# Kernel optimization log

Hardware: AMD Instinct MI355X
Metric: run time of the kernel (lower is better)

The kernel has to match this reference:

```python
import jax, jax.numpy as jnp
import numpy as np

N, E, DIM, L, NPERM, B = 20000, 640000, 128, 4, 20000, 256
R = NPERM * L * L  # rows of perm matrices
EPS = 1e-5


def _mlp(x, w1, b1, g, beta, w2, b2):
    # Linear -> BatchNorm (training-mode batch stats) -> ReLU -> Linear
    h = x @ w1 + b1
    mu = h.mean(0)
    var = h.var(0)  # biased, matches torch BN normalization
    h = (h - mu) * jax.lax.rsqrt(var + EPS) * g + beta
    return jax.nn.relu(h) @ w2 + b2


def setup_inputs() -> dict:
    key = jax.random.key(0)
    ks = jax.random.split(key, 40)
    s = 0.05
    inp = {}
    inp["node_feat"] = jax.random.normal(ks[0], (N, DIM), jnp.float32)
    inp["edge_feat"] = jax.random.normal(ks[1], (E, DIM), jnp.float32)
    inp["src"] = jax.random.randint(ks[2], (E,), 0, N)
    inp["dst"] = jax.random.randint(ks[3], (E,), 0, N)
    inp["rev_flag"] = jax.random.randint(ks[4], (E,), 0, 2).astype(bool)
    # sparse node_to_perm / edge_to_perm: one nnz per row (row i implicit)
    inp["n2p_cols"] = jax.random.randint(ks[5], (R,), 0, N)
    inp["n2p_vals"] = jax.random.uniform(ks[6], (R,), jnp.float32)
    inp["e2p_cols"] = jax.random.randint(ks[7], (R,), 0, E)
    inp["e2p_vals"] = jax.random.uniform(ks[8], (R,), jnp.float32)
    # sparse pooling matrix: perm j -> graph pool_rows[j] with weight pool_vals[j]
    inp["pool_rows"] = jax.random.randint(ks[9], (NPERM,), 0, B)
    inp["pool_vals"] = jax.random.uniform(ks[10], (NPERM,), jnp.float32)
    for i, n in enumerate(["in_w", "out_w", "src_w", "dst_w", "nloop_w", "eloop_w"]):
        inp[n] = jax.random.normal(ks[11 + i], (DIM, DIM), jnp.float32) * s
    inp["lrp_w"] = jax.random.normal(ks[17], (DIM, DIM, L * L), jnp.float32) * s
    inp["nbias"] = jnp.zeros((DIM,), jnp.float32)
    inp["ebias"] = jnp.zeros((DIM,), jnp.float32)
    inp["lrp_bias"] = jnp.zeros((DIM,), jnp.float32)
    for p, k0 in (("n", 20), ("e", 26)):
        inp[p + "mlp_w1"] = jax.random.normal(ks[k0], (DIM, DIM), jnp.float32) * s
        inp[p + "mlp_b1"] = jnp.zeros((DIM,), jnp.float32)
        inp[p + "mlp_g"] = jnp.ones((DIM,), jnp.float32)
        inp[p + "mlp_beta"] = jnp.zeros((DIM,), jnp.float32)
        inp[p + "mlp_w2"] = jax.random.normal(ks[k0 + 1], (DIM, DIM), jnp.float32) * s
        inp[p + "mlp_b2"] = jnp.zeros((DIM,), jnp.float32)
    return inp


def reference(node_feat, edge_feat, src, dst, rev_flag, n2p_cols, n2p_vals,
              e2p_cols, e2p_vals, pool_rows, pool_vals,
              in_w, out_w, src_w, dst_w, nloop_w, eloop_w, lrp_w,
              nbias, ebias, lrp_bias,
              nmlp_w1, nmlp_b1, nmlp_g, nmlp_beta, nmlp_w2, nmlp_b2,
              emlp_w1, emlp_b1, emlp_g, emlp_beta, emlp_w2, emlp_b2):
    hs = node_feat[src]   # [E, d]
    hd = node_feat[dst]   # [E, d]
    r = rev_flag[:, None]
    # per-edge messages with reverse-edge masking
    edge_msg = jnp.where(r, hs @ dst_w - hd @ src_w, hd @ dst_w - hs @ src_w)
    node_msg = jnp.where(r, edge_feat @ out_w, -(edge_feat @ in_w))
    node_agg = jax.ops.segment_sum(node_msg, dst, num_segments=N)
    # node update
    nout = _mlp(node_feat @ nloop_w + node_agg + nbias,
                nmlp_w1, nmlp_b1, nmlp_g, nmlp_beta, nmlp_w2, nmlp_b2)
    # edge update: degree-scaled term uses out-degree of dst node
    out_deg = jax.ops.segment_sum(jnp.ones((E,), jnp.float32), src, num_segments=N)
    dlog = jnp.log2(1.0 + out_deg[dst])[:, None]
    add = 2.0 * (1.0 + dlog) * (edge_feat @ (src_w - dst_w))
    eout = _mlp(edge_feat @ eloop_w + add + edge_msg + ebias,
                emlp_w1, emlp_b1, emlp_g, emlp_beta, emlp_w2, emlp_b2)
    # sparse perm gathers + LRP einsum + sparse pooling scatter
    perm = n2p_vals[:, None] * nout[n2p_cols] + e2p_vals[:, None] * eout[e2p_cols]
    perm = perm.reshape(NPERM, L * L, DIM)
    lrp = jnp.einsum('dab,bca->dc', perm, lrp_w) + lrp_bias
    pooled = jax.ops.segment_sum(pool_vals[:, None] * lrp, pool_rows, num_segments=B)
    return pooled, eout
```

## Files before the change

kernel.cpp:

```cpp
#include <hip/hip_runtime.h>
#include <stdint.h>

constexpr int Nn     = 20000;
constexpr int Ee     = 640000;
constexpr int NPERMc = 20000;

using bf16x8 = __attribute__((ext_vector_type(8))) short;
using f32x4  = __attribute__((ext_vector_type(4))) float;
using s16x4  = __attribute__((ext_vector_type(4))) short;
using u16x8  = __attribute__((ext_vector_type(8))) unsigned short;

__device__ __forceinline__ short f2bf(float f) {
  union { float f; unsigned u; } v; v.f = f;
  unsigned r = v.u + 0x7FFFu + ((v.u >> 16) & 1u);
  return (short)(r >> 16);
}
__device__ __forceinline__ float bf2f(unsigned short s) {
  union { unsigned u; float f; } v; v.u = ((unsigned)s) << 16;
  return v.f;
}
__device__ __forceinline__ f32x4 MFMA(bf16x8 a, bf16x8 b, f32x4 c) {
  return __builtin_amdgcn_mfma_f32_16x16x32_bf16(a, b, c, 0, 0, 0);
}

__device__ __forceinline__ int swz(int s) { return s ^ (((s >> 7) & 7) << 3); }

__device__ __forceinline__ int fragIdx(int k, int n) {
  int t = n >> 4, kk = k >> 5;
  int l = ((k & 31) >> 3) * 16 + (n & 15);
  int j = k & 7;
  return ((t * 4 + kk) * 64 + l) * 8 + j;
}

__device__ __forceinline__ void stage16x128(const float* __restrict__ src, int row0, int M,
                                            int lane, short* lds) {
  #pragma unroll
  for (int it = 0; it < 8; ++it) {
    int u = it * 64 + lane;
    int r = u >> 5;
    int q = u & 31;
    int row = row0 + r;
    float4 v = make_float4(0.f, 0.f, 0.f, 0.f);
    if (row < M) v = ((const float4*)(src + (size_t)row * 128))[q];
    int k  = q * 4;
    int kk = k >> 5;
    int l2 = ((k & 31) >> 3) * 16 + r;
    int j  = k & 7;
    s16x4 s4 = { f2bf(v.x), f2bf(v.y), f2bf(v.z), f2bf(v.w) };
    *(s16x4*)(lds + swz((kk * 64 + l2) * 8 + j)) = s4;
  }
}

__global__ __launch_bounds__(256) void kPrep(
    const float* __restrict__ in_w,  const float* __restrict__ out_w,
    const float* __restrict__ src_w, const float* __restrict__ dst_w,
    const float* __restrict__ nloop_w, const float* __restrict__ eloop_w,
    const float* __restrict__ lrp_w,
    const float* __restrict__ nbias, const float* __restrict__ ebias,
    const float* __restrict__ w1e, const float* __restrict__ b1e,
    const float* __restrict__ w1n, const float* __restrict__ b1n,
    const float* __restrict__ w2e, const float* __restrict__ w2n,
    short* __restrict__ WA, short* __restrict__ BQ, short* __restrict__ WN,
    short* __restrict__ W2E, short* __restrict__ W2N, short* __restrict__ WL,
    float* __restrict__ c0e, float* __restrict__ c0n) {
  __shared__ float Rl[16384];
  int tid = threadIdx.x;
  int blk = blockIdx.x;
  if (blk < 448) {
    int p = blk >> 6, sub = blk & 63;
    const float* La; const float* Lb = nullptr; const float* R; short* outp;
    float sOut = 1.f;
    switch (p) {
      case 0: La = eloop_w;             R = w1e; outp = WA;          break;
      case 1: La = src_w; Lb = dst_w;   R = w1e; outp = WA + 16384;  break;
      case 2: La = dst_w;               R = w1e; outp = BQ;          break;
      case 3: La = src_w;               R = w1e; outp = BQ + 16384;  break;
      case 4: La = nloop_w;             R = w1n; outp = WN;          break;
      case 5: La = out_w;               R = w1n; outp = WN + 16384;  break;
      default: La = in_w;               R = w1n; outp = WN + 32768; sOut = -1.f; break;
    }
    for (int i = tid; i < 16384; i += 256) Rl[i] = R[i];
    __syncthreads();
    int e = sub * 256 + tid;
    int k = e >> 7, n = e & 127;
    float acc = 0.f;
    bool hasLb = (Lb != nullptr);
    for (int j = 0; j < 128; ++j) {
      float l = La[k * 128 + j];
      if (hasLb) l -= Lb[k * 128 + j];
      acc += l * Rl[j * 128 + n];
    }
    outp[fragIdx(k, n)] = f2bf(acc * sOut);
  } else if (blk < 512) {
    int e = (blk - 448) * 256 + tid; int k = e >> 7, n = e & 127;
    W2E[fragIdx(k, n)] = f2bf(w2e[k * 128 + n]);
  } else if (blk < 576) {
    int e = (blk - 512) * 256 + tid; int k = e >> 7, n = e & 127;
    W2N[fragIdx(k, n)] = f2bf(w2n[k * 128 + n]);
  } else if (blk < 1600) {
    int q = blk - 576; int a = q >> 6;
    int e = (q & 63) * 256 + tid; int k = e >> 7, n = e & 127;
    WL[a * 16384 + fragIdx(k, n)] = f2bf(lrp_w[(k * 128 + n) * 16 + a]);
  } else {
    if (tid < 128) {
      float acc = 0.f;
      for (int k2 = 0; k2 < 128; ++k2) acc += ebias[k2] * w1e[k2 * 128 + tid];
      c0e[tid] = acc + b1e[tid];
    } else {
      int n = tid - 128; float acc = 0.f;
      for (int k2 = 0; k2 < 128; ++k2) acc += nbias[k2] * w1n[k2 * 128 + n];
      c0n[n] = acc + b1n[n];
    }
  }
}


__global__ __launch_bounds__(256) void kHist(
    const int* __restrict__ srcI, const int* __restrict__ dstI,
    int* __restrict__ cnt, float* __restrict__ deg) {
  int e = blockIdx.x * 256 + threadIdx.x;
  atomicAdd(&cnt[dstI[e]], 1);
  atomicAdd(&deg[srcI[e]], 1.0f);
}

__global__ __launch_bounds__(256) void kScan(const int* __restrict__ cnt,
                                             int* __restrict__ off,
                                             int* __restrict__ cur) {
  __shared__ int lc[Nn];
  __shared__ int ps[256];
  int tid = threadIdx.x;
  for (int i = tid; i < Nn; i += 256) lc[i] = cnt[i];
  __syncthreads();
  constexpr int CH = (Nn + 255) / 256;
  int base = tid * CH;
  int local = 0;
  for (int i = 0; i < CH; ++i) {
    int idx = base + i;
    if (idx < Nn) local += lc[idx];
  }
  ps[tid] = local;
  __syncthreads();
  for (int d = 1; d < 256; d <<= 1) {
    int t = (tid >= d) ? ps[tid - d] : 0;
    __syncthreads();
    if (tid >= d) ps[tid] += t;
    __syncthreads();
  }
  int run = ps[tid] - local;
  for (int i = 0; i < CH; ++i) {
    int idx = base + i;
    if (idx < Nn) { off[idx] = run; cur[idx] = run; run += lc[idx]; }
  }
}

__global__ __launch_bounds__(256) void kScatter(
    const int* __restrict__ dstI, const int* __restrict__ revI,
    int* __restrict__ cur, int* __restrict__ order) {
  int e = blockIdx.x * 256 + threadIdx.x;
  int pos = atomicAdd(&cur[dstI[e]], 1);
  order[pos] = revI[e] ? (e | (int)0x80000000) : e;
}

__global__ __launch_bounds__(256) void kAgg2(
    const float* __restrict__ ef, const int* __restrict__ off,
    const int* __restrict__ cnt, const int* __restrict__ order,
    float* __restrict__ aggR, float* __restrict__ aggN) {
  int w = threadIdx.x >> 6, lane = threadIdx.x & 63;
  int n = blockIdx.x * 4 + w;
  if (n >= Nn) return;
  int s0 = off[n], c = cnt[n];
  float2 aR = make_float2(0.f, 0.f), aN = make_float2(0.f, 0.f);
  int i = 0;
  for (; i + 3 < c; i += 4) {
    int oe0 = order[s0 + i];
    int oe1 = order[s0 + i + 1];
    int oe2 = order[s0 + i + 2];
    int oe3 = order[s0 + i + 3];
    float2 v0 = ((const float2*)(ef + (size_t)(oe0 & 0x7fffffff) * 128))[lane];
    float2 v1 = ((const float2*)(ef + (size_t)(oe1 & 0x7fffffff) * 128))[lane];
    float2 v2 = ((const float2*)(ef + (size_t)(oe2 & 0x7fffffff) * 128))[lane];
    float2 v3 = ((const float2*)(ef + (size_t)(oe3 & 0x7fffffff) * 128))[lane];
    if (oe0 < 0) { aR.x += v0.x; aR.y += v0.y; } else { aN.x += v0.x; aN.y += v0.y; }
    if (oe1 < 0) { aR.x += v1.x; aR.y += v1.y; } else { aN.x += v1.x; aN.y += v1.y; }
    if (oe2 < 0) { aR.x += v2.x; aR.y += v2.y; } else { aN.x += v2.x; aN.y += v2.y; }
    if (oe3 < 0) { aR.x += v3.x; aR.y += v3.y; } else { aN.x += v3.x; aN.y += v3.y; }
  }
  for (; i < c; ++i) {
    int oe = order[s0 + i];
    int e = oe & 0x7fffffff;
    float2 v = ((const float2*)(ef + (size_t)e * 128))[lane];
    if (oe < 0) { aR.x += v.x; aR.y += v.y; } else { aN.x += v.x; aN.y += v.y; }
  }
  ((float2*)(aggR + (size_t)n * 128))[lane] = aR;
  ((float2*)(aggN + (size_t)n * 128))[lane] = aN;
}

__global__ __launch_bounds__(256, 2) void kQ(const float* __restrict__ nf,
                                             const short* __restrict__ BQ,
                                             float* __restrict__ Q, int M) {
  __shared__ __align__(16) short alds[4][2048];
  __shared__ __align__(16) short wbuf[8192];
  int tid = threadIdx.x, w = tid >> 6, lane = tid & 63;
  int row0 = blockIdx.x * 64 + w * 16;
  stage16x128(nf, row0, M, lane, alds[w]);
  f32x4 acc[16];
  #pragma unroll
  for (int t = 0; t < 16; ++t) acc[t] = (f32x4){0.f, 0.f, 0.f, 0.f};
  const int4* g4 = (const int4*)BQ;
  for (int kk = 0; kk < 4; ++kk) {
    __syncthreads();
    for (int c = tid; c < 1024; c += 256) {
      int t = c >> 6, l = c & 63;
      ((int4*)wbuf)[c] = g4[(t * 4 + kk) * 64 + l];
    }
    __syncthreads();
    bf16x8 a = *(const bf16x8*)(alds[w] + swz((kk * 64 + lane) * 8));
    #pragma unroll
    for (int t = 0; t < 16; ++t) {
      bf16x8 b = *(const bf16x8*)(wbuf + (t * 64 + lane) * 8);
      acc[t] = MFMA(a, b, acc[t]);
    }
  }
  int sub = lane >> 4, m = lane & 15;
  #pragma unroll
  for (int i = 0; i < 4; ++i) {
    int row = row0 + sub * 4 + i;
    if (row < M) {
      #pragma unroll
      for (int h = 0; h < 2; ++h) {
        float4 f0, f1;
        f0.x = acc[h * 8 + 0][i]; f0.y = acc[h * 8 + 1][i];
        f0.z = acc[h * 8 + 2][i]; f0.w = acc[h * 8 + 3][i];
        f1.x = acc[h * 8 + 4][i]; f1.y = acc[h * 8 + 5][i];
        f1.z = acc[h * 8 + 6][i]; f1.w = acc[h * 8 + 7][i];
        float4* dst = (float4*)(Q + (size_t)row * 256 + h * 128 + m * 8);
        dst[0] = f0; dst[1] = f1;
      }
    }
  }
}

__global__ __launch_bounds__(256, 2) void kN1(
    const float* __restrict__ nf, const float* __restrict__ aggR,
    const float* __restrict__ aggN, const short* __restrict__ WN,
    const float* __restrict__ c0n, short* __restrict__ hN,
    float* __restrict__ scratchN, int M) {
  __shared__ __align__(16) short alds[4][2048];
  __shared__ __align__(16) short wlds[16384];
  __shared__ float statsLDS[256];
  int tid = threadIdx.x, w = tid >> 6, lane = tid & 63;
  int m = lane & 15, sub = lane >> 4;
  statsLDS[tid] = 0.f;
  int row0 = blockIdx.x * 64 + w * 16;
  f32x4 acc[8];
  #pragma unroll
  for (int t = 0; t < 8; ++t) acc[t] = (f32x4){0.f, 0.f, 0.f, 0.f};
  for (int s = 0; s < 3; ++s) {
    const float* src = (s == 0) ? nf : ((s == 1) ? aggR : aggN);
    __syncthreads();
    const int4* g4 = (const int4*)(WN + s * 16384);
    for (int c = tid; c < 2048; c += 256) ((int4*)wlds)[c] = g4[c];
    __syncthreads();
    stage16x128(src, row0, M, lane, alds[w]);
    for (int kk = 0; kk < 4; ++kk) {
      bf16x8 a = *(const bf16x8*)(alds[w] + swz((kk * 64 + lane) * 8));
      #pragma unroll
      for (int t = 0; t < 8; ++t) {
        bf16x8 b = *(const bf16x8*)(wlds + ((t * 4 + kk) * 64 + lane) * 8);
        acc[t] = MFMA(a, b, acc[t]);
      }
    }
  }
  float c0v[8];
  #pragma unroll
  for (int t = 0; t < 8; ++t) c0v[t] = c0n[t * 16 + m];
  float ss[8], sq[8];
  #pragma unroll
  for (int t = 0; t < 8; ++t) { ss[t] = 0.f; sq[t] = 0.f; }
  #pragma unroll
  for (int i = 0; i < 4; ++i) {
    int row = row0 + sub * 4 + i;
    if (row < M) {
      bf16x8 pk;
      #pragma unroll
      for (int t = 0; t < 8; ++t) {
        float h = acc[t][i] + c0v[t];
        pk[t] = f2bf(h); ss[t] += h; sq[t] += h * h;
      }
      *(bf16x8*)(hN + (size_t)row * 128 + m * 8) = pk;
    }
  }
  #pragma unroll
  for (int t = 0; t < 8; ++t) {
    float a = ss[t], b = sq[t];
    a += __shfl_xor(a, 16, 64); b += __shfl_xor(b, 16, 64);
    a += __shfl_xor(a, 32, 64); b += __shfl_xor(b, 32, 64);
    if (lane < 16) {
      atomicAdd(&statsLDS[t * 16 + lane], a);
      atomicAdd(&statsLDS[128 + t * 16 + lane], b);
    }
  }
  __syncthreads();
  scratchN[(size_t)blockIdx.x * 256 + tid] = statsLDS[tid];
}

__global__ __launch_bounds__(256, 4) void kD(
    const float* __restrict__ ef, const short* __restrict__ WA,
    const float* __restrict__ Q, const float* __restrict__ c0e,
    const int* __restrict__ srcI, const int* __restrict__ dstI,
    const int* __restrict__ revI, const float* __restrict__ deg,
    short* __restrict__ hE, float* __restrict__ scratchE) {
  __shared__ __align__(16) short alds[4][2048];
  __shared__ __align__(16) short wbuf[8192];
  __shared__ float statsLDS[256];
  int tid = threadIdx.x, w = tid >> 6, lane = tid & 63;
  int m = lane & 15, sub = lane >> 4;
  statsLDS[tid] = 0.f;
  int row0 = blockIdx.x * 64 + w * 16;
  float scl[4]; int qa[4], qb[4];
  #pragma unroll
  for (int i = 0; i < 4; ++i) {
    int e = row0 + sub * 4 + i;
    int s_ = srcI[e], d_ = dstI[e], r_ = revI[e];
    scl[i] = 2.0f * (1.0f + log2f(1.0f + deg[d_]));
    int na = r_ ? s_ : d_;
    int nb = r_ ? d_ : s_;
    qa[i] = na * 256 + m * 8;
    qb[i] = nb * 256 + 128 + m * 8;
  }
  stage16x128(ef, row0, Ee, lane, alds[w]);
  f32x4 acc1[8], acc2[8];
  #pragma unroll
  for (int t = 0; t < 8; ++t) { acc1[t] = (f32x4){0,0,0,0}; acc2[t] = (f32x4){0,0,0,0}; }
  const int4* g4 = (const int4*)WA;
  for (int kk = 0; kk < 4; ++kk) {
    __syncthreads();
    for (int c = tid; c < 1024; c += 256) {
      int mm = c >> 9, t = (c >> 6) & 7, l = c & 63;
      ((int4*)wbuf)[c] = g4[mm * 2048 + (t * 4 + kk) * 64 + l];
    }
    __syncthreads();
    bf16x8 a = *(const bf16x8*)(alds[w] + swz((kk * 64 + lane) * 8));
    #pragma unroll
    for (int t = 0; t < 8; ++t) {
      bf16x8 b1 = *(const bf16x8*)(wbuf + (t * 64 + lane) * 8);
      bf16x8 b2 = *(const bf16x8*)(wbuf + 4096 + (t * 64 + lane) * 8);
      acc1[t] = MFMA(a, b1, acc1[t]);
      acc2[t] = MFMA(a, b2, acc2[t]);
    }
  }
  float c0v[8];
  #pragma unroll
  for (int t = 0; t < 8; ++t) c0v[t] = c0e[t * 16 + m];
  float ss[8], sq[8];
  #pragma unroll
  for (int t = 0; t < 8; ++t) { ss[t] = 0.f; sq[t] = 0.f; }
  #pragma unroll
  for (int i = 0; i < 4; ++i) {
    int e = row0 + sub * 4 + i;
    float4 A0 = ((const float4*)(Q + qa[i]))[0];
    float4 A1 = ((const float4*)(Q + qa[i]))[1];
    float4 B0 = ((const float4*)(Q + qb[i]))[0];
    float4 B1 = ((const float4*)(Q + qb[i]))[1];
    float qv[8] = {A0.x - B0.x, A0.y - B0.y, A0.z - B0.z, A0.w - B0.w,
                   A1.x - B1.x, A1.y - B1.y, A1.z - B1.z, A1.w - B1.w};
    bf16x8 pk;
    #pragma unroll
    for (int t = 0; t < 8; ++t) {
      float h = acc1[t][i] + scl[i] * acc2[t][i] + qv[t] + c0v[t];
      pk[t] = f2bf(h);
      ss[t] += h; sq[t] += h * h;
    }
    *(bf16x8*)(hE + (size_t)e * 128 + m * 8) = pk;
  }
  #pragma unroll
  for (int t = 0; t < 8; ++t) {
    float a = ss[t], b = sq[t];
    a += __shfl_xor(a, 16, 64); b += __shfl_xor(b, 16, 64);
    a += __shfl_xor(a, 32, 64); b += __shfl_xor(b, 32, 64);
    if (lane < 16) {
      atomicAdd(&statsLDS[t * 16 + lane], a);
      atomicAdd(&statsLDS[128 + t * 16 + lane], b);
    }
  }
  __syncthreads();
  scratchE[(size_t)blockIdx.x * 256 + tid] = statsLDS[tid];
}

__global__ __launch_bounds__(256) void kRed(const float* __restrict__ scr, int NB,
                                            float* __restrict__ part) {
  int tid = threadIdx.x, b = blockIdx.x;
  float acc = 0.f;
  for (int r = b; r < NB; r += 64)
    acc += scr[(size_t)r * 256 + tid];
  part[b * 256 + tid] = acc;
}

__global__ __launch_bounds__(256) void kFin(const float* __restrict__ part,
                                            float M, const float* __restrict__ g,
                                            const float* __restrict__ beta,
                                            float* __restrict__ st) {
  __shared__ float red[256];
  __shared__ float red2[256];
  int c = blockIdx.x;
  int tid = threadIdx.x;
  float s = 0.f, q = 0.f;
  if (tid < 64) {
    s = part[tid * 256 + c];
    q = part[tid * 256 + 128 + c];
  }
  red[tid] = s; red2[tid] = q;
  __syncthreads();
  for (int off = 32; off > 0; off >>= 1) {
    if (tid < off) { red[tid] += red[tid + off]; red2[tid] += red2[tid + off]; }
    __syncthreads();
  }
  if (tid == 0) {
    float mu  = red[0] / M;
    float var = red2[0] / M - mu * mu;
    float inv = rsqrtf(var + 1e-5f);
    float sc  = g[c] * inv;
    st[c] = sc;
    st[128 + c] = beta[c] - mu * sc;
  }
}

__global__ __launch_bounds__(256, 6) void kF(const short* __restrict__ h,
                                             const float* __restrict__ st,
                                             const short* __restrict__ w2f,
                                             const float* __restrict__ b2,
                                             float* __restrict__ outp, int M) {
  __shared__ __align__(16) short alds[4][2048];
  __shared__ __align__(16) short wbuf[4096];
  int tid = threadIdx.x, w = tid >> 6, lane = tid & 63;
  int m2 = lane & 15;
  int row0 = blockIdx.x * 64 + w * 16;
  float sc8[8], tb8[8];
  #pragma unroll
  for (int q = 0; q < 8; ++q) {
    int col = q * 16 + m2;
    sc8[q] = st[col]; tb8[q] = st[128 + col];
  }
  #pragma unroll
  for (int it = 0; it < 4; ++it) {
    int r = it * 4 + (lane >> 4);
    int row = row0 + r;
    u16x8 hv = {0, 0, 0, 0, 0, 0, 0, 0};
    if (row < M) hv = *(const u16x8*)(h + (size_t)row * 128 + m2 * 8);
    #pragma unroll
    for (int q = 0; q < 8; ++q) {
      float f = bf2f(hv[q]);
      float v = fmaxf(f * sc8[q] + tb8[q], 0.f);
      int k = q * 16 + m2;
      int kk = k >> 5, l2 = ((k & 31) >> 3) * 16 + r, j = k & 7;
      alds[w][swz((kk * 64 + l2) * 8 + j)] = f2bf(v);
    }
  }
  f32x4 acc[8];
  #pragma unroll
  for (int t = 0; t < 8; ++t) acc[t] = (f32x4){0.f, 0.f, 0.f, 0.f};
  const int4* g4w = (const int4*)w2f;
  for (int kk = 0; kk < 4; ++kk) {
    __syncthreads();
    for (int c = tid; c < 512; c += 256) {
      int t = c >> 6, l = c & 63;
      ((int4*)wbuf)[c] = g4w[(t * 4 + kk) * 64 + l];
    }
    __syncthreads();
    bf16x8 a = *(const bf16x8*)(alds[w] + swz((kk * 64 + lane) * 8));
    #pragma unroll
    for (int t = 0; t < 8; ++t) {
      bf16x8 b = *(const bf16x8*)(wbuf + (t * 64 + lane) * 8);
      acc[t] = MFMA(a, b, acc[t]);
    }
  }
  int sub = lane >> 4;
  #pragma unroll
  for (int t = 0; t < 8; ++t) {
    int col = t * 16 + (lane & 15);
    float bb = b2[col];
    #pragma unroll
    for (int i = 0; i < 4; ++i) {
      int row = row0 + sub * 4 + i;
      if (row < M) outp[(size_t)row * 128 + col] = acc[t][i] + bb;
    }
  }
}

__global__ __launch_bounds__(256, 4) void kLRP(
    const float* __restrict__ nout, const float* __restrict__ eoutp,
    const int* __restrict__ n2pc, const float* __restrict__ n2pv,
    const int* __restrict__ e2pc, const float* __restrict__ e2pv,
    const int* __restrict__ poolr, const float* __restrict__ poolv,
    const short* __restrict__ WL, const float* __restrict__ lrp_bias,
    float* __restrict__ pooled) {
  __shared__ __align__(16) short alds[4][2048];
  __shared__ __align__(16) short wbuf[4096];
  int tid = threadIdx.x, w = tid >> 6, lane = tid & 63;
  int blk = blockIdx.x % 313, g = blockIdx.x / 313;
  int row0 = blk * 64 + w * 16;
  int a0 = g * 4;
  f32x4 acc[8];
  #pragma unroll
  for (int t = 0; t < 8; ++t) acc[t] = (f32x4){0.f, 0.f, 0.f, 0.f};
  for (int a = a0; a < a0 + 4; ++a) {
    #pragma unroll
    for (int it = 0; it < 8; ++it) {
      int u = it * 64 + lane;
      int r = u >> 5;
      int q = u & 31;
      int d = row0 + r;
      float4 v = make_float4(0.f, 0.f, 0.f, 0.f);
      if (d < NPERMc) {
        int i = d * 16 + a;
        int nc = n2pc[i]; float nv = n2pv[i];
        int ec = e2pc[i]; float ev = e2pv[i];
        float4 nr = ((const float4*)(nout  + (size_t)nc * 128))[q];
        float4 er = ((const float4*)(eoutp + (size_t)ec * 128))[q];
        v.x = nv * nr.x + ev * er.x;
        v.y = nv * nr.y + ev * er.y;
        v.z = nv * nr.z + ev * er.z;
        v.w = nv * nr.w + ev * er.w;
      }
      int k  = q * 4;
      int kk = k >> 5;
      int l2 = ((k & 31) >> 3) * 16 + r;
      int j  = k & 7;
      s16x4 s4 = { f2bf(v.x), f2bf(v.y), f2bf(v.z), f2bf(v.w) };
      *(s16x4*)(alds[w] + swz((kk * 64 + l2) * 8 + j)) = s4;
    }
    const int4* g4 = (const int4*)(WL + a * 16384);
    for (int kk = 0; kk < 4; ++kk) {
      __syncthreads();
      for (int c = tid; c < 512; c += 256) {
        int t = c >> 6, l = c & 63;
        ((int4*)wbuf)[c] = g4[(t * 4 + kk) * 64 + l];
      }
      __syncthreads();
      bf16x8 aa = *(const bf16x8*)(alds[w] + swz((kk * 64 + lane) * 8));
      #pragma unroll
      for (int t = 0; t < 8; ++t) {
        bf16x8 b = *(const bf16x8*)(wbuf + (t * 64 + lane) * 8);
        acc[t] = MFMA(aa, b, acc[t]);
      }
    }
  }
  int sub = lane >> 4;
  #pragma unroll
  for (int t = 0; t < 8; ++t) {
    int col = t * 16 + (lane & 15);
    float lb = (g == 0) ? lrp_bias[col] : 0.f;
    #pragma unroll
    for (int i = 0; i < 4; ++i) {
      int d = row0 + sub * 4 + i;
      if (d < NPERMc) {
        float val = acc[t][i] + lb;
        atomicAdd(&pooled[poolr[d] * 128 + col], poolv[d] * val);
      }
    }
  }
}

extern "C" void kernel_launch(void* const* d_in, const int* in_sizes, int n_in,
                              void* d_out, int out_size, void* d_ws, size_t ws_size,
                              hipStream_t stream) {
  (void)in_sizes; (void)n_in; (void)out_size; (void)ws_size;
  const float* node_feat = (const float*)d_in[0];
  const float* edge_feat = (const float*)d_in[1];
  const int*   srcI      = (const int*)d_in[2];
  const int*   dstI      = (const int*)d_in[3];
  const int*   revI      = (const int*)d_in[4];
  const int*   n2pc      = (const int*)d_in[5];
  const float* n2pv      = (const float*)d_in[6];
  const int*   e2pc      = (const int*)d_in[7];
  const float* e2pv      = (const float*)d_in[8];
  const int*   poolr     = (const int*)d_in[9];
  const float* poolv     = (const float*)d_in[10];
  const float* in_w      = (const float*)d_in[11];
  const float* out_w     = (const float*)d_in[12];
  const float* src_w     = (const float*)d_in[13];
  const float* dst_w     = (const float*)d_in[14];
  const float* nloop_w   = (const float*)d_in[15];
  const float* eloop_w   = (const float*)d_in[16];
  const float* lrp_w     = (const float*)d_in[17];
  const float* nbias     = (const float*)d_in[18];
  const float* ebias     = (const float*)d_in[19];
  const float* lrp_bias  = (const float*)d_in[20];
  const float* nmlp_w1   = (const float*)d_in[21];
  const float* nmlp_b1   = (const float*)d_in[22];
  const float* nmlp_g    = (const float*)d_in[23];
  const float* nmlp_beta = (const float*)d_in[24];
  const float* nmlp_w2   = (const float*)d_in[25];
  const float* nmlp_b2   = (const float*)d_in[26];
  const float* emlp_w1   = (const float*)d_in[27];
  const float* emlp_b1   = (const float*)d_in[28];
  const float* emlp_g    = (const float*)d_in[29];
  const float* emlp_beta = (const float*)d_in[30];
  const float* emlp_w2   = (const float*)d_in[31];
  const float* emlp_b2   = (const float*)d_in[32];

  float* pooled = (float*)d_out;
  float* eoutp  = (float*)d_out + 32768;

  char* p = (char*)d_ws;
  auto alloc = [&](size_t b) { char* r = p; p += (b + 255) & ~(size_t)255; return r; };
  short* hE   = (short*)alloc((size_t)Ee * 128 * 2);
  float* Qm   = (float*)alloc((size_t)Nn * 256 * 4);
  float* aggR = (float*)alloc((size_t)Nn * 128 * 4);
  float* aggN = (float*)alloc((size_t)Nn * 128 * 4);
  short* hN   = (short*)alloc((size_t)Nn * 128 * 2);
  float* nout = (float*)alloc((size_t)Nn * 128 * 4);
  float* deg  = (float*)alloc((size_t)Nn * 4);
  float* scrE = (float*)alloc((size_t)10000 * 256 * 4);
  float* scrN = (float*)alloc((size_t)313 * 256 * 4);
  float* partE= (float*)alloc((size_t)64 * 256 * 4);
  float* partN= (float*)alloc((size_t)64 * 256 * 4);
  float* stE  = (float*)alloc(256 * 4);
  float* stN  = (float*)alloc(256 * 4);
  short* WA   = (short*)alloc(32768 * 2);
  short* BQ   = (short*)alloc(32768 * 2);
  short* WN   = (short*)alloc(49152 * 2);
  short* W2E  = (short*)alloc(16384 * 2);
  short* W2N  = (short*)alloc(16384 * 2);
  short* WL   = (short*)alloc((size_t)16 * 16384 * 2);
  float* c0e  = (float*)alloc(128 * 4);
  float* c0n  = (float*)alloc(128 * 4);
  int*   cnt  = (int*)alloc((size_t)Nn * 4);
  int*   offA = (int*)alloc((size_t)Nn * 4);
  int*   cur  = (int*)alloc((size_t)Nn * 4);
  int*   order= (int*)alloc((size_t)Ee * 4);

  hipMemsetAsync(deg,  0, (size_t)Nn * 4, stream);
  hipMemsetAsync(cnt,  0, (size_t)Nn * 4, stream);
  hipMemsetAsync(pooled, 0, (size_t)32768 * 4, stream);

  kPrep<<<1601, 256, 0, stream>>>(in_w, out_w, src_w, dst_w, nloop_w, eloop_w, lrp_w,
                                  nbias, ebias, emlp_w1, emlp_b1, nmlp_w1, nmlp_b1,
                                  emlp_w2, nmlp_w2, WA, BQ, WN, W2E, W2N, WL, c0e, c0n);
  kHist<<<Ee / 256, 256, 0, stream>>>(srcI, dstI, cnt, deg);
  kScan<<<1, 256, 0, stream>>>(cnt, offA, cur);
  kScatter<<<Ee / 256, 256, 0, stream>>>(dstI, revI, cur, order);
  kAgg2<<<Nn / 4, 256, 0, stream>>>(edge_feat, offA, cnt, order, aggR, aggN);
  kQ<<<313, 256, 0, stream>>>(node_feat, BQ, Qm, Nn);
  kN1<<<313, 256, 0, stream>>>(node_feat, aggR, aggN, WN, c0n, hN, scrN, Nn);
  kD<<<10000, 256, 0, stream>>>(edge_feat, WA, Qm, c0e, srcI, dstI, revI, deg, hE, scrE);
  kRed<<<64, 256, 0, stream>>>(scrE, 10000, partE);
  kRed<<<64, 256, 0, stream>>>(scrN, 313, partN);
  kFin<<<128, 256, 0, stream>>>(partE, (float)Ee, emlp_g, emlp_beta, stE);
  kFin<<<128, 256, 0, stream>>>(partN, (float)Nn, nmlp_g, nmlp_beta, stN);
  kF<<<10000, 256, 0, stream>>>(hE, stE, W2E, emlp_b2, eoutp, Ee);
  kF<<<313, 256, 0, stream>>>(hN, stN, W2N, nmlp_b2, nout, Nn);
  kLRP<<<1252, 256, 0, stream>>>(nout, eoutp, n2pc, n2pv, e2pc, e2pv,
                                 poolr, poolv, WL, lrp_bias, pooled);
}
```

Measured before the change: 1.306 ms.

## Store Q in bf16, precompute edge degree scale, stage full LRP weights once

```diff
diff --git a/kernel.cpp b/kernel.cpp
--- a/kernel.cpp
+++ b/kernel.cpp
@@ -155,10 +155,13 @@
 
 __global__ __launch_bounds__(256) void kScatter(
     const int* __restrict__ dstI, const int* __restrict__ revI,
-    int* __restrict__ cur, int* __restrict__ order) {
+    int* __restrict__ cur, int* __restrict__ order,
+    const float* __restrict__ deg, float* __restrict__ sclE) {
   int e = blockIdx.x * 256 + threadIdx.x;
-  int pos = atomicAdd(&cur[dstI[e]], 1);
+  int d = dstI[e];
+  int pos = atomicAdd(&cur[d], 1);
   order[pos] = revI[e] ? (e | (int)0x80000000) : e;
+  sclE[e] = 2.0f * (1.0f + log2f(1.0f + deg[d]));
 }
 
 __global__ __launch_bounds__(256) void kAgg2(
@@ -197,7 +200,7 @@
 
 __global__ __launch_bounds__(256, 2) void kQ(const float* __restrict__ nf,
                                              const short* __restrict__ BQ,
-                                             float* __restrict__ Q, int M) {
+                                             short* __restrict__ Qb, int M) {
   __shared__ __align__(16) short alds[4][2048];
   __shared__ __align__(16) short wbuf[8192];
   int tid = threadIdx.x, w = tid >> 6, lane = tid & 63;
@@ -228,13 +231,10 @@
     if (row < M) {
       #pragma unroll
       for (int h = 0; h < 2; ++h) {
-        float4 f0, f1;
-        f0.x = acc[h * 8 + 0][i]; f0.y = acc[h * 8 + 1][i];
-        f0.z = acc[h * 8 + 2][i]; f0.w = acc[h * 8 + 3][i];
-        f1.x = acc[h * 8 + 4][i]; f1.y = acc[h * 8 + 5][i];
-        f1.z = acc[h * 8 + 6][i]; f1.w = acc[h * 8 + 7][i];
-        float4* dst = (float4*)(Q + (size_t)row * 256 + h * 128 + m * 8);
-        dst[0] = f0; dst[1] = f1;
+        bf16x8 pk;
+        #pragma unroll
+        for (int tt = 0; tt < 8; ++tt) pk[tt] = f2bf(acc[h * 8 + tt][i]);
+        *(bf16x8*)(Qb + (size_t)row * 256 + h * 128 + m * 8) = pk;
       }
     }
   }
@@ -306,9 +306,9 @@
 
 __global__ __launch_bounds__(256, 4) void kD(
     const float* __restrict__ ef, const short* __restrict__ WA,
-    const float* __restrict__ Q, const float* __restrict__ c0e,
+    const short* __restrict__ Qb, const float* __restrict__ c0e,
     const int* __restrict__ srcI, const int* __restrict__ dstI,
-    const int* __restrict__ revI, const float* __restrict__ deg,
+    const int* __restrict__ revI, const float* __restrict__ sclE,
     short* __restrict__ hE, float* __restrict__ scratchE) {
   __shared__ __align__(16) short alds[4][2048];
   __shared__ __align__(16) short wbuf[8192];
@@ -322,7 +322,7 @@
   for (int i = 0; i < 4; ++i) {
     int e = row0 + sub * 4 + i;
     int s_ = srcI[e], d_ = dstI[e], r_ = revI[e];
-    scl[i] = 2.0f * (1.0f + log2f(1.0f + deg[d_]));
+    scl[i] = sclE[e];
     int na = r_ ? s_ : d_;
     int nb = r_ ? d_ : s_;
     qa[i] = na * 256 + m * 8;
@@ -358,16 +358,13 @@
   #pragma unroll
   for (int i = 0; i < 4; ++i) {
     int e = row0 + sub * 4 + i;
-    float4 A0 = ((const float4*)(Q + qa[i]))[0];
-    float4 A1 = ((const float4*)(Q + qa[i]))[1];
-    float4 B0 = ((const float4*)(Q + qb[i]))[0];
-    float4 B1 = ((const float4*)(Q + qb[i]))[1];
-    float qv[8] = {A0.x - B0.x, A0.y - B0.y, A0.z - B0.z, A0.w - B0.w,
-                   A1.x - B1.x, A1.y - B1.y, A1.z - B1.z, A1.w - B1.w};
+    u16x8 A = *(const u16x8*)(Qb + qa[i]);
+    u16x8 B = *(const u16x8*)(Qb + qb[i]);
     bf16x8 pk;
     #pragma unroll
     for (int t = 0; t < 8; ++t) {
-      float h = acc1[t][i] + scl[i] * acc2[t][i] + qv[t] + c0v[t];
+      float qv = bf2f(A[t]) - bf2f(B[t]);
+      float h = acc1[t][i] + scl[i] * acc2[t][i] + qv + c0v[t];
       pk[t] = f2bf(h);
       ss[t] += h; sq[t] += h * h;
     }
@@ -487,7 +484,7 @@
   }
 }
 
-__global__ __launch_bounds__(256, 4) void kLRP(
+__global__ __launch_bounds__(256, 2) void kLRP(
     const float* __restrict__ nout, const float* __restrict__ eoutp,
     const int* __restrict__ n2pc, const float* __restrict__ n2pv,
     const int* __restrict__ e2pc, const float* __restrict__ e2pv,
@@ -495,7 +492,7 @@
     const short* __restrict__ WL, const float* __restrict__ lrp_bias,
     float* __restrict__ pooled) {
   __shared__ __align__(16) short alds[4][2048];
-  __shared__ __align__(16) short wbuf[4096];
+  __shared__ __align__(16) short wlds[16384];
   int tid = threadIdx.x, w = tid >> 6, lane = tid & 63;
   int blk = blockIdx.x % 313, g = blockIdx.x / 313;
   int row0 = blk * 64 + w * 16;
@@ -504,6 +501,10 @@
   #pragma unroll
   for (int t = 0; t < 8; ++t) acc[t] = (f32x4){0.f, 0.f, 0.f, 0.f};
   for (int a = a0; a < a0 + 4; ++a) {
+    __syncthreads();
+    const int4* g4 = (const int4*)(WL + a * 16384);
+    for (int c = tid; c < 2048; c += 256) ((int4*)wlds)[c] = g4[c];
+    __syncthreads();
     #pragma unroll
     for (int it = 0; it < 8; ++it) {
       int u = it * 64 + lane;
@@ -529,18 +530,11 @@
       s16x4 s4 = { f2bf(v.x), f2bf(v.y), f2bf(v.z), f2bf(v.w) };
       *(s16x4*)(alds[w] + swz((kk * 64 + l2) * 8 + j)) = s4;
     }
-    const int4* g4 = (const int4*)(WL + a * 16384);
     for (int kk = 0; kk < 4; ++kk) {
-      __syncthreads();
-      for (int c = tid; c < 512; c += 256) {
-        int t = c >> 6, l = c & 63;
-        ((int4*)wbuf)[c] = g4[(t * 4 + kk) * 64 + l];
-      }
-      __syncthreads();
       bf16x8 aa = *(const bf16x8*)(alds[w] + swz((kk * 64 + lane) * 8));
       #pragma unroll
       for (int t = 0; t < 8; ++t) {
-        bf16x8 b = *(const bf16x8*)(wbuf + (t * 64 + lane) * 8);
+        bf16x8 b = *(const bf16x8*)(wlds + ((t * 4 + kk) * 64 + lane) * 8);
         acc[t] = MFMA(aa, b, acc[t]);
       }
     }
@@ -605,7 +599,7 @@
   char* p = (char*)d_ws;
   auto alloc = [&](size_t b) { char* r = p; p += (b + 255) & ~(size_t)255; return r; };
   short* hE   = (short*)alloc((size_t)Ee * 128 * 2);
-  float* Qm   = (float*)alloc((size_t)Nn * 256 * 4);
+  short* Qb   = (short*)alloc((size_t)Nn * 256 * 2);
   float* aggR = (float*)alloc((size_t)Nn * 128 * 4);
   float* aggN = (float*)alloc((size_t)Nn * 128 * 4);
   short* hN   = (short*)alloc((size_t)Nn * 128 * 2);
@@ -629,6 +623,7 @@
   int*   offA = (int*)alloc((size_t)Nn * 4);
   int*   cur  = (int*)alloc((size_t)Nn * 4);
   int*   order= (int*)alloc((size_t)Ee * 4);
+  float* sclE = (float*)alloc((size_t)Ee * 4);
 
   hipMemsetAsync(deg,  0, (size_t)Nn * 4, stream);
   hipMemsetAsync(cnt,  0, (size_t)Nn * 4, stream);
@@ -639,11 +634,11 @@
                                   emlp_w2, nmlp_w2, WA, BQ, WN, W2E, W2N, WL, c0e, c0n);
   kHist<<<Ee / 256, 256, 0, stream>>>(srcI, dstI, cnt, deg);
   kScan<<<1, 256, 0, stream>>>(cnt, offA, cur);
-  kScatter<<<Ee / 256, 256, 0, stream>>>(dstI, revI, cur, order);
+  kScatter<<<Ee / 256, 256, 0, stream>>>(dstI, revI, cur, order, deg, sclE);
   kAgg2<<<Nn / 4, 256, 0, stream>>>(edge_feat, offA, cnt, order, aggR, aggN);
-  kQ<<<313, 256, 0, stream>>>(node_feat, BQ, Qm, Nn);
+  kQ<<<313, 256, 0, stream>>>(node_feat, BQ, Qb, Nn);
   kN1<<<313, 256, 0, stream>>>(node_feat, aggR, aggN, WN, c0n, hN, scrN, Nn);
-  kD<<<10000, 256, 0, stream>>>(edge_feat, WA, Qm, c0e, srcI, dstI, revI, deg, hE, scrE);
+  kD<<<10000, 256, 0, stream>>>(edge_feat, WA, Qb, c0e, srcI, dstI, revI, sclE, hE, scrE);
   kRed<<<64, 256, 0, stream>>>(scrE, 10000, partE);
   kRed<<<64, 256, 0, stream>>>(scrN, 313, partN);
   kFin<<<128, 256, 0, stream>>>(partE, (float)Ee, emlp_g, emlp_beta, stE);
```

New measurement: 1.300 ms, median of 2. No clear change (-0.5%).
